# Kernel tuning notes

Hardware: AMD Instinct MI355X
Metric: run time of the kernel (lower is better)

The kernel has to match this reference:

```python
import jax, jax.numpy as jnp
import numpy as np

B, T, C, D = 16, 2048, 1024, 128  # batch, seq, n_embd, head_size

def setup_inputs() -> dict:
    key = jax.random.key(0)
    kx, kq, kk, kv = jax.random.split(key, 4)
    x = jax.random.normal(kx, (B, T, C), dtype=jnp.float32)
    s = 1.0 / np.sqrt(C)
    Wq = jax.random.normal(kq, (C, D), dtype=jnp.float32) * s
    Wk = jax.random.normal(kk, (C, D), dtype=jnp.float32) * s
    Wv = jax.random.normal(kv, (C, D), dtype=jnp.float32) * s
    return {"x": x, "Wq": Wq, "Wk": Wk, "Wv": Wv}

def reference(x, Wq, Wk, Wv):
    # q,k,v: [B,T,D]
    q = jnp.einsum('btc,cd->btd', x, Wq)
    k = jnp.einsum('btc,cd->btd', x, Wk)
    v = jnp.einsum('btc,cd->btd', x, Wv)
    scale = 1.0 / jnp.sqrt(jnp.asarray(q.shape[-1], q.dtype))
    wei = jnp.einsum('bqd,bkd->bqk', q, k) * scale  # [B,T,T]
    causal = jnp.tril(jnp.ones((T, T), dtype=bool))
    wei = jnp.where(causal, wei, -jnp.inf)
    wei = jax.nn.softmax(wei, axis=-1)
    # dropout is identity in eval mode
    out = jnp.einsum('bqk,bkd->bqd', wei, v)  # [B,T,D]
    return out
```

## Files before the change

### kernel.cpp

```cpp
#include <hip/hip_runtime.h>

typedef unsigned short u16;
typedef unsigned int   u32;
typedef __attribute__((ext_vector_type(8)))  __bf16 bf16x8;
typedef __attribute__((ext_vector_type(16))) float  f32x16;
typedef __attribute__((ext_vector_type(4)))  float  fl4;
typedef __attribute__((ext_vector_type(4)))  u16    u16x4;
typedef __attribute__((ext_vector_type(4)))  u32    u32x4;

#define NB 16
#define NT 2048
#define NC 1024
#define ND 128


__device__ __forceinline__ u16 f2bf(float f) {
  u32 u = __builtin_bit_cast(u32, f);
  u = (u + 0x7fffu + ((u >> 16) & 1u)) >> 16;
  return (u16)u;
}

__device__ __forceinline__ u32 pk2(float lo, float hi) {
  return (u32)f2bf(lo) | ((u32)f2bf(hi) << 16);
}

__global__ __launch_bounds__(256) void wprep_k(
    const float* __restrict__ Wq, const float* __restrict__ Wk,
    const float* __restrict__ Wv, u16* __restrict__ wf)
{
  const int cb   = blockIdx.x;
  const int kind = cb >> 2;
  const float* __restrict__ W = (kind == 0) ? Wq : (kind == 1) ? Wk : Wv;
  const int lane = threadIdx.x & 63;
  const int ksq  = threadIdx.x >> 6;
  const int l31 = lane & 31, hi = lane >> 5;
  const int d = (cb & 3) * 32 + l31;
  u16* __restrict__ o = wf + (size_t)cb * 64 * 512;
  #pragma unroll 4
  for (int ii = 0; ii < 16; ++ii) {
    int ks = ksq * 16 + ii;
    int k  = ks * 16 + hi * 8;
    u16x4 p0, p1;
    #pragma unroll
    for (int j = 0; j < 4; ++j) p0[j] = f2bf(W[(size_t)(k + j) * ND + d]);
    #pragma unroll
    for (int j = 0; j < 4; ++j) p1[j] = f2bf(W[(size_t)(k + 4 + j) * ND + d]);
    u16* dst = o + ((size_t)ks * 64 + lane) * 8;
    *(u16x4*)dst = p0;
    *(u16x4*)(dst + 4) = p1;
  }
}

__global__ __launch_bounds__(512, 4) void qkv_fused_k(
    const float* __restrict__ x, const u16* __restrict__ wf,
    u16* __restrict__ qf, u16* __restrict__ kf, u16* __restrict__ vf)
{
  const int blk  = blockIdx.x;
  const int brow = blk >> 1;
  const int h    = blk & 1;
  const int tid  = threadIdx.x;
  const int lane = tid & 63;
  const int wid  = tid >> 6;
  const int rw = wid & 3, cw = wid >> 2;
  const int l31 = lane & 31, hi = lane >> 5;
  const int m0 = brow * 128;
  const int cbg0 = h * 6;

  __shared__ u16 Ab[2][16 * 512];
  __shared__ u16 Bb[2][24 * 512];

  const int arow = tid & 127;
  const int ac   = tid >> 7;
  const float* __restrict__ xr = x + (size_t)(m0 + arow) * NC;
  const int ad0 = ((ac >> 1) * 4 + (arow >> 5)) * 64 + (arow & 31) + 32 * (ac & 1);
  const int ac4 = ac + 4;
  const int ad1 = ((ac4 >> 1) * 4 + (arow >> 5)) * 64 + (arow & 31) + 32 * (ac4 & 1);

  fl4 xa, xb, xc, xd;
  bf16x8 bw[3];

  auto issueA = [&](int bk) {
    const float* p = xr + bk * 64 + ac * 8;
    xa = *(const fl4*)(p);
    xb = *(const fl4*)(p + 4);
    xc = *(const fl4*)(p + 32);
    xd = *(const fl4*)(p + 36);
  };
  auto issueB = [&](int bk) {
    #pragma unroll
    for (int i = 0; i < 3; ++i) {
      int idx = i * 512 + tid;
      int cb6 = idx >> 8, ks = (idx >> 6) & 3;
      bw[i] = *(const bf16x8*)(wf + (((size_t)(cbg0 + cb6) * 64 + bk * 4 + ks) * 64 + (idx & 63)) * 8);
    }
  };
  auto writeA = [&](int buf) {
    bf16x8 v0, v1;
    v0[0]=(__bf16)xa[0]; v0[1]=(__bf16)xa[1]; v0[2]=(__bf16)xa[2]; v0[3]=(__bf16)xa[3];
    v0[4]=(__bf16)xb[0]; v0[5]=(__bf16)xb[1]; v0[6]=(__bf16)xb[2]; v0[7]=(__bf16)xb[3];
    v1[0]=(__bf16)xc[0]; v1[1]=(__bf16)xc[1]; v1[2]=(__bf16)xc[2]; v1[3]=(__bf16)xc[3];
    v1[4]=(__bf16)xd[0]; v1[5]=(__bf16)xd[1]; v1[6]=(__bf16)xd[2]; v1[7]=(__bf16)xd[3];
    *(bf16x8*)&Ab[buf][(size_t)ad0 * 8] = v0;
    *(bf16x8*)&Ab[buf][(size_t)ad1 * 8] = v1;
  };
  auto writeB = [&](int buf) {
    #pragma unroll
    for (int i = 0; i < 3; ++i)
      *(bf16x8*)&Bb[buf][((size_t)i * 512 + tid) * 8] = bw[i];
  };

  f32x16 acc[3] = {};

  issueA(0); issueB(0);
  writeA(0); writeB(0);
  __syncthreads();

  for (int bk = 0; bk < 16; ++bk) {
    const int cur = bk & 1;
    if (bk < 15) { issueA(bk + 1); issueB(bk + 1); }
    #pragma unroll
    for (int ks = 0; ks < 4; ++ks) {
      bf16x8 a = *(const bf16x8*)&Ab[cur][((size_t)(ks * 4 + rw) * 64 + lane) * 8];
      #pragma unroll
      for (int cb = 0; cb < 3; ++cb) {
        bf16x8 b = *(const bf16x8*)&Bb[cur][((size_t)((cw * 3 + cb) * 4 + ks) * 64 + lane) * 8];
        acc[cb] = __builtin_amdgcn_mfma_f32_32x32x16_bf16(a, b, acc[cb], 0, 0, 0);
      }
    }
    if (bk < 15) { writeA(cur ^ 1); writeB(cur ^ 1); }
    __syncthreads();
  }

  const int t32 = brow * 4 + rw;
  #pragma unroll
  for (int cb = 0; cb < 3; ++cb) {
    const int colb = h * 192 + cw * 96 + cb * 32;
    const int kind = colb >> 7;
    const int d    = (colb & 127) + l31;
    if (kind < 2) {
      u16* __restrict__ o = kind ? kf : qf;
      const float sc = kind ? 1.0f : 0.12752539240377073f;
      const int ds = d >> 4, b3 = (d >> 3) & 1, j = d & 7;
      u16* __restrict__ base = o + ((size_t)t32 * 8 + ds) * 512 + 32 * b3 * 8 + j;
      #pragma unroll
      for (int r = 0; r < 16; ++r) {
        int crow = (r & 3) + 8 * (r >> 2) + 4 * hi;
        base[crow * 8] = f2bf(acc[cb][r] * sc);
      }
    } else {
      const int dt = (d & 127) >> 5;
      #pragma unroll
      for (int g = 0; g < 4; ++g) {
        int c16   = t32 * 2 + (g >> 1);
        int lanep = l31 + 32 * (g & 1);
        u16x4 pk;
        #pragma unroll
        for (int jj = 0; jj < 4; ++jj) pk[jj] = f2bf(acc[cb][g * 4 + jj]);
        *(u16x4*)(vf + (((size_t)c16 * 4 + dt) * 64 + lanep) * 8 + 4 * hi) = pk;
      }
    }
  }
}

__global__ __launch_bounds__(128, 2) void attn_fwd_k(
    const u16* __restrict__ qw, const u16* __restrict__ kw,
    const u16* __restrict__ vw, float* __restrict__ out)
{
  const int tid  = threadIdx.x;
  const int lane = tid & 63;
  const int w    = tid >> 6;
  const int l31  = lane & 31;
  const int hi   = lane >> 5;

  const int c  = blockIdx.x;
  const int bb = (c >> 6) & 15;
  const int qi = ((c & 63) + ((c >> 8) << 4)) & 63;
  const int q0 = qi * 32;
  const int qrow = q0 + l31;

  const u16* __restrict__ qb = qw + ((size_t)bb * 64 + qi) * 4096;
  const u16* __restrict__ kb = kw + (size_t)bb * 64 * 4096;
  const u16* __restrict__ vb = vw + (size_t)bb * 128 * 2048;

  __shared__ float ofs[64][64];
  __shared__ float mls[2][64];

  bf16x8 qfr[8];
  #pragma unroll
  for (int s = 0; s < 8; ++s)
    qfr[s] = *(const bf16x8*)(qb + ((size_t)s * 64 + lane) * 8);

  f32x16 of[4] = {};
  float m_run = -__builtin_inff();
  float l_run = 0.f;

  const int nsteps = (qi >> 1) + 1;
  for (int s = w; s < nsteps; s += 2) {
    const int kv0 = s * 64;
    const bool masked = (s == nsteps - 1);

    bf16x8 kf0[8], kf1[8];
    #pragma unroll
    for (int t = 0; t < 8; ++t) {
      kf0[t] = *(const bf16x8*)(kb + (((size_t)(2 * s) * 8 + t) * 64 + lane) * 8);
      kf1[t] = *(const bf16x8*)(kb + (((size_t)(2 * s + 1) * 8 + t) * 64 + lane) * 8);
    }
    f32x16 st0 = {}, st1 = {};
    #pragma unroll
    for (int t = 0; t < 8; ++t) {
      st0 = __builtin_amdgcn_mfma_f32_32x32x16_bf16(kf0[t], qfr[t], st0, 0, 0, 0);
      st1 = __builtin_amdgcn_mfma_f32_32x32x16_bf16(kf1[t], qfr[t], st1, 0, 0, 0);
    }
    bf16x8 vfr[4][4];
    #pragma unroll
    for (int ks = 0; ks < 4; ++ks)
      #pragma unroll
      for (int dt = 0; dt < 4; ++dt)
        vfr[dt][ks] = *(const bf16x8*)(vb + (((size_t)((kv0 >> 4) + ks) * 4 + dt) * 64 + lane) * 8);

    if (masked) {
      #pragma unroll
      for (int r = 0; r < 16; ++r) {
        int crow = (r & 3) + 8 * (r >> 2) + 4 * hi;
        st0[r] = (kv0 + crow      <= qrow) ? st0[r] : -1e30f;
        st1[r] = (kv0 + 32 + crow <= qrow) ? st1[r] : -1e30f;
      }
    }

    float pmax = -1e30f;
    #pragma unroll
    for (int r = 0; r < 16; ++r) pmax = fmaxf(pmax, fmaxf(st0[r], st1[r]));
    pmax = fmaxf(pmax, __shfl_xor(pmax, 32, 64));

    const bool no_rescale = (pmax <= m_run);
    const float m_new = fmaxf(m_run, pmax);
    const float fac = __builtin_amdgcn_exp2f(m_run - m_new);
    float rsum = 0.f;
    #pragma unroll
    for (int r = 0; r < 16; ++r) {
      st0[r] = __builtin_amdgcn_exp2f(st0[r] - m_new);
      st1[r] = __builtin_amdgcn_exp2f(st1[r] - m_new);
      rsum += st0[r] + st1[r];
    }
    rsum += __shfl_xor(rsum, 32, 64);
    l_run = l_run * fac + rsum;
    m_run = m_new;

    if (!__all(no_rescale)) {
      #pragma unroll
      for (int r = 0; r < 16; ++r) {
        float fr = __shfl(fac, (r & 3) + 8 * (r >> 2) + 4 * hi, 64);
        #pragma unroll
        for (int dt = 0; dt < 4; ++dt) of[dt][r] *= fr;
      }
    }

    u32x4 pa[4];
    #pragma unroll
    for (int g = 0; g < 4; ++g) {
      const float* sp = (g < 2) ? (const float*)&st0 : (const float*)&st1;
      const int o8 = (g & 1) * 8;
      u32 a0 = pk2(sp[o8 + 0], sp[o8 + 1]);
      u32 a1 = pk2(sp[o8 + 2], sp[o8 + 3]);
      u32 b0 = pk2(sp[o8 + 4], sp[o8 + 5]);
      u32 b1 = pk2(sp[o8 + 6], sp[o8 + 7]);
      u32 ta0 = __shfl_xor(a0, 32, 64);
      u32 ta1 = __shfl_xor(a1, 32, 64);
      u32 tb0 = __shfl_xor(b0, 32, 64);
      u32 tb1 = __shfl_xor(b1, 32, 64);
      pa[g][0] = hi ? tb0 : a0;
      pa[g][1] = hi ? tb1 : a1;
      pa[g][2] = hi ? b0  : ta0;
      pa[g][3] = hi ? b1  : ta1;
    }

    #pragma unroll
    for (int ks = 0; ks < 4; ++ks) {
      bf16x8 paf = __builtin_bit_cast(bf16x8, pa[ks]);
      #pragma unroll
      for (int dt = 0; dt < 4; ++dt)
        of[dt] = __builtin_amdgcn_mfma_f32_32x32x16_bf16(paf, vfr[dt][ks], of[dt], 0, 0, 0);
    }
  }

  if (w == 1) {
    #pragma unroll
    for (int dt = 0; dt < 4; ++dt)
      #pragma unroll
      for (int r = 0; r < 16; ++r)
        ofs[dt * 16 + r][lane] = of[dt][r];
    mls[0][lane] = m_run;
    mls[1][lane] = l_run;
  }
  __syncthreads();
  if (w == 0) {
    const float m1 = mls[0][l31];
    const float l1 = mls[1][l31];
    const float mt = fmaxf(m_run, m1);
    const float f0 = __builtin_amdgcn_exp2f(m_run - mt);
    const float f1 = __builtin_amdgcn_exp2f(m1 - mt);
    const float lt = l_run * f0 + l1 * f1;
    const float rl = 1.0f / lt;
    #pragma unroll
    for (int r = 0; r < 16; ++r) {
      int crow = (r & 3) + 8 * (r >> 2) + 4 * hi;
      float f0r = __shfl(f0, crow, 64);
      float f1r = __shfl(f1, crow, 64);
      float lr  = __shfl(rl, crow, 64);
      #pragma unroll
      for (int dt = 0; dt < 4; ++dt)
        out[((size_t)(bb * NT + q0 + crow)) * ND + dt * 32 + l31] =
            (of[dt][r] * f0r + ofs[dt * 16 + r][lane] * f1r) * lr;
    }
  }
}

extern "C" void kernel_launch(void* const* d_in, const int* in_sizes, int n_in,
                              void* d_out, int out_size, void* d_ws, size_t ws_size,
                              hipStream_t stream) {
  (void)in_sizes; (void)n_in; (void)out_size; (void)ws_size;
  const float* x  = (const float*)d_in[0];
  const float* Wq = (const float*)d_in[1];
  const float* Wk = (const float*)d_in[2];
  const float* Wv = (const float*)d_in[3];
  float* out = (float*)d_out;

  u16* qws = (u16*)d_ws;
  u16* kws = qws + (size_t)NB * NT * ND;
  u16* vws = kws + (size_t)NB * NT * ND;
  u16* wfs = vws + (size_t)NB * NT * ND;

  wprep_k<<<dim3(12), dim3(256), 0, stream>>>(Wq, Wk, Wv, wfs);
  qkv_fused_k<<<dim3(512), dim3(512), 0, stream>>>(x, wfs, qws, kws, vws);
  attn_fwd_k<<<dim3(1024), dim3(128), 0, stream>>>(qws, kws, vws, out);
}
```

Before: 119.1 us.

## Deepen x prefetch to two stages and use swizzled row-major LDS for A

The QKV projection kernel now keeps two register sets of x prefetched two k-blocks ahead instead of one. The main loop is unrolled by pairs so the register buffers ping-pong. The A tile in LDS moves from the MFMA-fragment layout to a row-major layout with an XOR swizzle, loaded with coalesced 16-byte rows per thread group. This aims to hide more global-load latency and improve coalescing of x reads, at the cost of more registers, which may reduce occupancy.

```diff
diff --git a/kernel.cpp b/kernel.cpp
--- a/kernel.cpp
+++ b/kernel.cpp
@@ -66,69 +66,78 @@
   const int m0 = brow * 128;
   const int cbg0 = h * 6;
 
-  __shared__ u16 Ab[2][16 * 512];
+  __shared__ u16 Ab[2][128 * 64];
   __shared__ u16 Bb[2][24 * 512];
 
-  const int arow = tid & 127;
-  const int ac   = tid >> 7;
-  const float* __restrict__ xr = x + (size_t)(m0 + arow) * NC;
-  const int ad0 = ((ac >> 1) * 4 + (arow >> 5)) * 64 + (arow & 31) + 32 * (ac & 1);
-  const int ac4 = ac + 4;
-  const int ad1 = ((ac4 >> 1) * 4 + (arow >> 5)) * 64 + (arow & 31) + 32 * (ac4 & 1);
-
-  fl4 xa, xb, xc, xd;
-  bf16x8 bw[3];
-
-  auto issueA = [&](int bk) {
-    const float* p = xr + bk * 64 + ac * 8;
-    xa = *(const fl4*)(p);
-    xb = *(const fl4*)(p + 4);
-    xc = *(const fl4*)(p + 32);
-    xd = *(const fl4*)(p + 36);
+  const int arow = tid >> 4;
+  const int ac4  = (tid & 15) * 4;
+  const float* __restrict__ xr = x + (size_t)(m0 + arow) * NC + ac4;
+
+  fl4 pA0[4], pA1[4];
+  bf16x8 pb[3];
+
+  auto issueA = [&](fl4* dst, int bk) {
+    #pragma unroll
+    for (int p = 0; p < 4; ++p)
+      dst[p] = *(const fl4*)(xr + (size_t)p * 32 * NC + bk * 64);
   };
   auto issueB = [&](int bk) {
     #pragma unroll
     for (int i = 0; i < 3; ++i) {
       int idx = i * 512 + tid;
       int cb6 = idx >> 8, ks = (idx >> 6) & 3;
-      bw[i] = *(const bf16x8*)(wf + (((size_t)(cbg0 + cb6) * 64 + bk * 4 + ks) * 64 + (idx & 63)) * 8);
-    }
-  };
-  auto writeA = [&](int buf) {
-    bf16x8 v0, v1;
-    v0[0]=(__bf16)xa[0]; v0[1]=(__bf16)xa[1]; v0[2]=(__bf16)xa[2]; v0[3]=(__bf16)xa[3];
-    v0[4]=(__bf16)xb[0]; v0[5]=(__bf16)xb[1]; v0[6]=(__bf16)xb[2]; v0[7]=(__bf16)xb[3];
-    v1[0]=(__bf16)xc[0]; v1[1]=(__bf16)xc[1]; v1[2]=(__bf16)xc[2]; v1[3]=(__bf16)xc[3];
-    v1[4]=(__bf16)xd[0]; v1[5]=(__bf16)xd[1]; v1[6]=(__bf16)xd[2]; v1[7]=(__bf16)xd[3];
-    *(bf16x8*)&Ab[buf][(size_t)ad0 * 8] = v0;
-    *(bf16x8*)&Ab[buf][(size_t)ad1 * 8] = v1;
+      pb[i] = *(const bf16x8*)(wf + (((size_t)(cbg0 + cb6) * 64 + bk * 4 + ks) * 64 + (idx & 63)) * 8);
+    }
+  };
+  auto writeA = [&](int buf, fl4* src) {
+    char* b = (char*)Ab[buf];
+    #pragma unroll
+    for (int p = 0; p < 4; ++p) {
+      int row = p * 32 + arow;
+      u16x4 pk;
+      pk[0] = f2bf(src[p][0]); pk[1] = f2bf(src[p][1]);
+      pk[2] = f2bf(src[p][2]); pk[3] = f2bf(src[p][3]);
+      *(u16x4*)(b + row * 128 + ((ac4 * 2) ^ ((row & 7) << 4))) = pk;
+    }
   };
   auto writeB = [&](int buf) {
     #pragma unroll
     for (int i = 0; i < 3; ++i)
-      *(bf16x8*)&Bb[buf][((size_t)i * 512 + tid) * 8] = bw[i];
+      *(bf16x8*)&Bb[buf][((size_t)i * 512 + tid) * 8] = pb[i];
   };
 
   f32x16 acc[3] = {};
 
-  issueA(0); issueB(0);
-  writeA(0); writeB(0);
+  auto compute = [&](int buf) {
+    const char* ab = (const char*)Ab[buf];
+    #pragma unroll
+    for (int ks = 0; ks < 4; ++ks) {
+      int row = rw * 32 + l31;
+      bf16x8 a = *(const bf16x8*)(ab + row * 128 + ((ks * 32 + hi * 16) ^ ((row & 7) << 4)));
+      #pragma unroll
+      for (int cb = 0; cb < 3; ++cb) {
+        bf16x8 b = *(const bf16x8*)&Bb[buf][((size_t)((cw * 3 + cb) * 4 + ks) * 64 + lane) * 8];
+        acc[cb] = __builtin_amdgcn_mfma_f32_32x32x16_bf16(a, b, acc[cb], 0, 0, 0);
+      }
+    }
+  };
+
+  auto ITER = [&](int bk, fl4* sFill, fl4* sNext) {
+    if (bk + 2 < 16) issueA(sFill, bk + 2);
+    if (bk + 1 < 16) issueB(bk + 1);
+    compute(bk & 1);
+    if (bk + 1 < 16) { writeA((bk + 1) & 1, sNext); writeB((bk + 1) & 1); }
+    __syncthreads();
+  };
+
+  issueA(pA0, 0); issueA(pA1, 1); issueB(0);
+  writeA(0, pA0); writeB(0);
   __syncthreads();
 
-  for (int bk = 0; bk < 16; ++bk) {
-    const int cur = bk & 1;
-    if (bk < 15) { issueA(bk + 1); issueB(bk + 1); }
-    #pragma unroll
-    for (int ks = 0; ks < 4; ++ks) {
-      bf16x8 a = *(const bf16x8*)&Ab[cur][((size_t)(ks * 4 + rw) * 64 + lane) * 8];
-      #pragma unroll
-      for (int cb = 0; cb < 3; ++cb) {
-        bf16x8 b = *(const bf16x8*)&Bb[cur][((size_t)((cw * 3 + cb) * 4 + ks) * 64 + lane) * 8];
-        acc[cb] = __builtin_amdgcn_mfma_f32_32x32x16_bf16(a, b, acc[cb], 0, 0, 0);
-      }
-    }
-    if (bk < 15) { writeA(cur ^ 1); writeB(cur ^ 1); }
-    __syncthreads();
+  #pragma unroll
+  for (int i = 0; i < 8; ++i) {
+    ITER(2 * i,     pA0, pA1);
+    ITER(2 * i + 1, pA1, pA0);
   }
 
   const int t32 = brow * 4 + rw;
```

Result: faster. 102.5 us (-13.9%).
